# Optimization experiments

Hardware: AMD Instinct MI355X
Metric: run time of the kernel (lower is better)

Reference implementation:

```python
import jax, jax.numpy as jnp
import numpy as np

NMS_THRE = 0.4
NEG = -1e30  # sentinel for sort key of suppressed boxes


def _iou_adjacency(boxes, nms_thre):
    # boxes: [N,4] in cxcywh -> xyxy, then dense IoU >= thre adjacency (no self loops)
    cx, cy, w, h = boxes[:, 0], boxes[:, 1], boxes[:, 2], boxes[:, 3]
    x1 = cx - w / 2
    y1 = cy - h / 2
    x2 = x1 + w
    y2 = y1 + h
    b = jnp.stack([x1, y1, x2, y2], axis=-1)  # [N,4]
    area = (x2 - x1) * (y2 - y1)
    lt = jnp.maximum(b[:, None, :2], b[None, :, :2])  # [N,N,2]
    rb = jnp.minimum(b[:, None, 2:], b[None, :, 2:])
    wh = jnp.clip(rb - lt, 0.0)
    inter = wh[..., 0] * wh[..., 1]
    iou = inter / (area[:, None] + area[None, :] - inter)
    n = boxes.shape[0]
    return (iou >= nms_thre) & (~jnp.eye(n, dtype=bool))


def _greedy_suppress(valid0, adj, scores):
    # Sequential greedy NMS over candidates in descending score order.
    # valid shrinks monotonically, and valid <= valid0 always, so clearing
    # neighbors via adj row exactly matches the torch loop (which only clears
    # neighbors that were initially valid -- already-false entries are no-ops).
    order = jnp.argsort(-scores)

    def body(k, valid):
        idx = order[k]
        return jnp.where(valid[idx], valid & (~adj[idx]), valid)

    return jax.lax.fori_loop(0, scores.shape[0], body, valid0)


def _per_class(pro_c, con_c, conf_c, adj):
    # scatter_max over adjacency: max of con over neighbors (0 if no neighbors,
    # matching torch_scatter's zero-init)
    adj_con = jnp.max(jnp.where(adj, con_c[None, :], 0.0), axis=1)
    valid0 = (pro_c >= conf_c) & (pro_c >= adj_con) & (pro_c >= con_c)
    return _greedy_suppress(valid0, adj, pro_c)


def _per_image(pro, con, boxes, scale, conf_thres):
    # pro/con: [N,C]; boxes: [N,4] cxcywh; scale: scalar; conf_thres: [C]
    adj = _iou_adjacency(boxes, NMS_THRE)
    survive = jax.vmap(_per_class, in_axes=(1, 1, 0, None))(pro, con, conf_thres, adj)  # [C,N]
    b = boxes * scale
    cx, cy, w, h = b[:, 0], b[:, 1], b[:, 2], b[:, 3]
    xyxy = jnp.stack([cx - 0.5 * w, cy - 0.5 * h, cx + 0.5 * w, cy + 0.5 * h], axis=-1)  # [N,4]
    scores = pro.T  # [C,N]
    C = scores.shape[0]
    bws = jnp.concatenate(
        [jnp.broadcast_to(xyxy[None], (C,) + xyxy.shape), scores[..., None]], axis=-1
    )  # [C,N,5]
    bws = bws * survive[..., None].astype(bws.dtype)  # zero out suppressed rows
    key = jnp.where(survive, scores, NEG)
    perm = jnp.argsort(-key, axis=1)  # per-class descending score order
    bws = jnp.take_along_axis(bws, perm[..., None], axis=1)
    mask = jnp.take_along_axis(survive, perm, axis=1)
    return bws, mask


def setup_inputs() -> dict:
    key = jax.random.key(0)
    k1, k2, k3, k4 = jax.random.split(key, 4)
    B, N, C = 4, 3600, 16
    return {
        "pro_max": jax.random.uniform(k1, (B, N, C), dtype=jnp.float32),
        "con_max": jax.random.uniform(k2, (B, N, C), dtype=jnp.float32),
        "pred_boxes": jax.random.uniform(k3, (B, N, 4), dtype=jnp.float32),
        "image_scales": jax.random.uniform(k4, (B,), dtype=jnp.float32),
        "conf_thres": jnp.zeros((C,), dtype=jnp.float32),
    }


def reference(pro_max, con_max, pred_boxes, image_scales, conf_thres):
    # Returns (boxes_with_scores [B,C,N,5] sorted per class by score desc,
    #          survive_mask [B,C,N] aligned with the sorted rows).
    return jax.vmap(_per_image, in_axes=(0, 0, 0, 0, None))(
        pro_max, con_max, pred_boxes, image_scales, conf_thres
    )
```

## Files before the change

### kernel.cpp

```cpp
#include <hip/hip_runtime.h>
#include <cstdint>

typedef unsigned long long u64;
typedef unsigned int u32;

#define B_ 4
#define N_ 3600
#define C_ 16
#define NW_ 57
#define NPAD_ 3648
#define RPW_ 4
#define RPB_ 16
#define TPI_ 1596
#define HW0_ 1856
#define HW1_ 1792
#define CH_ 64
#define NTC_ 1024
#define NWVC_ 16
#define RPWGC_ 4

__global__ __launch_bounds__(256, 4) void k_adj(const float* __restrict__ boxes,
                                                u64* __restrict__ adj) {
#pragma clang fp contract(off)
    __shared__ float4 sbox[HW0_];
    const int tid  = threadIdx.x;
    const int lane = tid & 63;
    const int wv   = tid >> 6;
    const int g    = blockIdx.x;
    const int b    = g / (N_ / RPB_);
    const int rg   = g % (N_ / RPB_);
    const int r0   = rg * RPB_ + wv * RPW_;
    const int w0   = rg >> 2;
    const size_t bN = (size_t)b * N_;

    float4 bi[RPW_];
    float  ai[RPW_];
#pragma unroll
    for (int r = 0; r < RPW_; ++r) {
        const float4 bx = reinterpret_cast<const float4*>(boxes)[bN + r0 + r];
        const float x1 = bx.x - bx.z * 0.5f;
        const float y1 = bx.y - bx.w * 0.5f;
        const float x2 = x1 + bx.z;
        const float y2 = y1 + bx.w;
        bi[r] = make_float4(x1, y1, x2, y2);
        ai[r] = (x2 - x1) * (y2 - y1);
    }
    const double MID = (double)0.4f - 0x1p-26;

    u64 row[RPW_];
#pragma unroll
    for (int r = 0; r < RPW_; ++r) row[r] = 0ull;

    int jbase = 0;
    for (int h = 0; h < 2; ++h) {
        const int cnt  = h ? HW1_ : HW0_;
        const int wlo  = jbase >> 6;
        const int wcnt = cnt >> 6;
        if (w0 < wlo + wcnt) {
            const int tw0 = max(w0 - wlo, 0);
            const int jj0 = tw0 << 6;
            __syncthreads();
            for (int jj = jj0 + tid; jj < cnt; jj += 256) {
                const int j = jbase + jj;
                float x1 = 0.f, y1 = 0.f, x2 = 0.f, y2 = 0.f;
                if (j < N_) {
                    const float4 bx = reinterpret_cast<const float4*>(boxes)[bN + j];
                    x1 = bx.x - bx.z * 0.5f;
                    y1 = bx.y - bx.w * 0.5f;
                    x2 = x1 + bx.z;
                    y2 = y1 + bx.w;
                }
                sbox[jj] = make_float4(x1, y1, x2, y2);
            }
            __syncthreads();

            for (int tw = tw0; tw < wcnt; ++tw) {
                const int tglob = wlo + tw;
                const float4 bj = sbox[tw * 64 + lane];
                const float ajr = (bj.z - bj.x) * (bj.w - bj.y);
#pragma unroll
                for (int r = 0; r < RPW_; ++r) {
                    const float ltx = fmaxf(bi[r].x, bj.x);
                    const float lty = fmaxf(bi[r].y, bj.y);
                    const float rbx = fminf(bi[r].z, bj.z);
                    const float rby = fminf(bi[r].w, bj.w);
                    const float whx = fmaxf(rbx - ltx, 0.0f);
                    const float why = fmaxf(rby - lty, 0.0f);
                    const float inter = whx * why;
                    const float denom = (ai[r] + ajr) - inter;
                    const int pred = ((double)inter > MID * (double)denom);
                    const u64 m = __ballot(pred);
                    if (lane == tglob) row[r] = m;
                }
            }
        }
        jbase += cnt;
    }

#pragma unroll
    for (int r = 0; r < RPW_; ++r)
        if (lane == w0) row[r] &= ~(1ull << ((r0 + r) & 63));
#pragma unroll
    for (int r = 0; r < RPW_; ++r)
        if (lane >= w0 && lane < NW_)
            adj[(bN + r0 + r) * (size_t)NW_ + lane] = row[r];
}

__global__ __launch_bounds__(256) void k_tr(u64* __restrict__ adj,
                                            u32* __restrict__ cnt) {
    if (blockIdx.x == 0) {
        for (int x = threadIdx.x; x < B_ * C_ * 16; x += 256) cnt[x] = 0;
    }
    const int lane = threadIdx.x & 63;
    const int wv   = threadIdx.x >> 6;
    const int p    = blockIdx.x * 4 + wv;
    const int b    = p / TPI_;
    const int p2   = p % TPI_;
    int wi = (int)((1.0f + sqrtf((float)(8 * p2 + 1))) * 0.5f);
    while (wi * (wi - 1) / 2 > p2) --wi;
    while ((wi + 1) * wi / 2 <= p2) ++wi;
    const int wj = p2 - wi * (wi - 1) / 2;
    const size_t bN = (size_t)b * N_;

    u64 x = adj[(bN + wj * 64 + lane) * (size_t)NW_ + wi];

    const u64 M[6] = {0x00000000FFFFFFFFull, 0x0000FFFF0000FFFFull,
                      0x00FF00FF00FF00FFull, 0x0F0F0F0F0F0F0F0Full,
                      0x3333333333333333ull, 0x5555555555555555ull};
#pragma unroll
    for (int si = 0; si < 6; ++si) {
        const int s = 32 >> si;
        const u64 m = M[si];
        const u64 t = __shfl_xor(x, s);
        x = ((lane & s) == 0) ? ((x & m) | ((t & m) << s))
                              : ((x & ~m) | ((t & ~m) >> s));
    }
    const int rowi = wi * 64 + lane;
    if (rowi < N_)
        adj[(bN + rowi) * (size_t)NW_ + wj] = x;
}

__global__ __launch_bounds__(256) void k_acon(const u64* __restrict__ adj,
                                              const float* __restrict__ con,
                                              const float* __restrict__ pro,
                                              const float* __restrict__ conf,
                                              u64* __restrict__ cand,
                                              u32* __restrict__ cnt) {
    const int tid  = threadIdx.x;
    const int lane = tid & 63;
    const int wv   = tid >> 6;
    const int g    = blockIdx.x;
    const int b    = g / (N_ / 4);
    const int i    = (g % (N_ / 4)) * 4 + wv;
    const size_t bN = (size_t)b * N_;

    u64 w = (lane < NW_) ? adj[(bN + i) * (size_t)NW_ + lane] : 0ull;

    float cm[C_];
#pragma unroll
    for (int k = 0; k < C_; ++k) cm[k] = 0.0f;

    while (w) {
        const int bit = __builtin_ctzll(w); w &= w - 1;
        const int j   = lane * 64 + bit;
        const float4* cp = reinterpret_cast<const float4*>(con + (bN + j) * C_);
        const float4 c0 = cp[0], c1 = cp[1], c2 = cp[2], c3 = cp[3];
        cm[0]  = fmaxf(cm[0],  c0.x); cm[1]  = fmaxf(cm[1],  c0.y);
        cm[2]  = fmaxf(cm[2],  c0.z); cm[3]  = fmaxf(cm[3],  c0.w);
        cm[4]  = fmaxf(cm[4],  c1.x); cm[5]  = fmaxf(cm[5],  c1.y);
        cm[6]  = fmaxf(cm[6],  c1.z); cm[7]  = fmaxf(cm[7],  c1.w);
        cm[8]  = fmaxf(cm[8],  c2.x); cm[9]  = fmaxf(cm[9],  c2.y);
        cm[10] = fmaxf(cm[10], c2.z); cm[11] = fmaxf(cm[11], c2.w);
        cm[12] = fmaxf(cm[12], c3.x); cm[13] = fmaxf(cm[13], c3.y);
        cm[14] = fmaxf(cm[14], c3.z); cm[15] = fmaxf(cm[15], c3.w);
    }

#pragma unroll
    for (int off = 1; off < 64; off <<= 1) {
#pragma unroll
        for (int k = 0; k < C_; ++k) cm[k] = fmaxf(cm[k], __shfl_xor(cm[k], off));
    }
    if (lane == 0) {
        const float4* cp = reinterpret_cast<const float4*>(con + (bN + i) * C_);
        const float4 c0 = cp[0], c1 = cp[1], c2 = cp[2], c3 = cp[3];
        const float4* pp = reinterpret_cast<const float4*>(pro + (bN + i) * C_);
        const float4 p0 = pp[0], p1 = pp[1], p2 = pp[2], p3 = pp[3];
        const float4* fp = reinterpret_cast<const float4*>(conf);
        const float4 f0 = fp[0], f1 = fp[1], f2 = fp[2], f3 = fp[3];
        const float th[C_] = {
            fmaxf(cm[0],  c0.x), fmaxf(cm[1],  c0.y),
            fmaxf(cm[2],  c0.z), fmaxf(cm[3],  c0.w),
            fmaxf(cm[4],  c1.x), fmaxf(cm[5],  c1.y),
            fmaxf(cm[6],  c1.z), fmaxf(cm[7],  c1.w),
            fmaxf(cm[8],  c2.x), fmaxf(cm[9],  c2.y),
            fmaxf(cm[10], c2.z), fmaxf(cm[11], c2.w),
            fmaxf(cm[12], c3.x), fmaxf(cm[13], c3.y),
            fmaxf(cm[14], c3.z), fmaxf(cm[15], c3.w)};
        const float pr[C_] = {p0.x, p0.y, p0.z, p0.w, p1.x, p1.y, p1.z, p1.w,
                              p2.x, p2.y, p2.z, p2.w, p3.x, p3.y, p3.z, p3.w};
        const float cf[C_] = {f0.x, f0.y, f0.z, f0.w, f1.x, f1.y, f1.z, f1.w,
                              f2.x, f2.y, f2.z, f2.w, f3.x, f3.y, f3.z, f3.w};
#pragma unroll
        for (int k = 0; k < C_; ++k) {
            if (pr[k] >= cf[k] && pr[k] >= th[k]) {
                const u32 pb = __float_as_uint(pr[k]);
                const u32 pk = pb ^ ((pb >> 31) ? 0xFFFFFFFFu : 0x80000000u);
                const u32 pos = atomicAdd(&cnt[(b * C_ + k) * 16], 1u);
                cand[(size_t)(b * C_ + k) * N_ + pos] =
                    (((u64)(~pk)) << 32) | (u32)i;
            }
        }
    }
}

union OvT {
    u64 keys[NPAD_];
    u64 srows[2][CH_][NW_];
};

__global__ __launch_bounds__(NTC_) void k_nms_core(const u64* __restrict__ cand,
                                                   const u32* __restrict__ cnt,
                                                   const u64* __restrict__ adj,
                                                   u32* __restrict__ scnt,
                                                   u32* __restrict__ sl,
                                                   float* __restrict__ sf) {
#pragma clang fp contract(off)
    __shared__ OvT ov;
    __shared__ u32 sidx[NPAD_];
    __shared__ float sscore[NPAD_];
    __shared__ u64 sintra[CH_];
    __shared__ u64 vmask[NW_];
    __shared__ u64 s_accept;
    __shared__ u32 slist[NPAD_];
    __shared__ float slistf[NPAD_];
    __shared__ u32 s_S;
    const int tid  = threadIdx.x;
    const int lane = tid & 63;
    const int wv   = tid >> 6;
    const int bc   = blockIdx.x;
    const int b    = bc / C_;
    const size_t bN = (size_t)b * N_;

    const int T  = (int)cnt[bc * 16];
    const int TW = (T + 63) >> 6;
    for (int x = tid; x < TW * 64; x += NTC_)
        ov.keys[x] = (x < T) ? cand[(size_t)bc * N_ + x] : ~0ull;
    if (tid < NW_) vmask[tid] = 0ull;
    __syncthreads();

    for (int xp = 0; xp * NTC_ < T; ++xp) {
        const int x  = xp * NTC_ + tid;
        const u64 kx = (x < T) ? ov.keys[x] : ~0ull;
        u32 rank = 0;
        if (x < TW * 64) {
            for (int yb = 0; yb < TW; ++yb) {
                const u64 ky = ov.keys[yb * 64 + lane];
                const u32 kyl = (u32)ky, kyh = (u32)(ky >> 32);
#pragma unroll
                for (int l = 0; l < 64; ++l) {
                    const u64 kb =
                        ((u64)(u32)__builtin_amdgcn_readlane((int)kyh, l) << 32)
                      |  (u64)(u32)__builtin_amdgcn_readlane((int)kyl, l);
                    rank += (kb < kx) ? 1u : 0u;
                }
            }
        }
        if (x < T) {
            const u32 i = (u32)(kx & 0xFFFFFFFFull);
            sidx[rank] = i;
            const u32 pk = ~((u32)(kx >> 32));
            const u32 pb = (pk & 0x80000000u) ? (pk ^ 0x80000000u) : ~pk;
            sscore[rank] = __uint_as_float(pb);
            atomicOr(&vmask[i >> 6], 1ull << (i & 63));
        }
    }
    __syncthreads();

#pragma unroll
    for (int rr = 0; rr < RPWGC_; ++rr) {
        const int r = wv * RPWGC_ + rr;
        const u32 idx = (r < T) ? sidx[r] : 0u;
        if (lane < NW_)
            ov.srows[0][r][lane] = adj[(bN + idx) * (size_t)NW_ + lane];
    }
    __syncthreads();

    u32 S = 0;
    const int NCH = (T + CH_ - 1) / CH_;
    for (int ch = 0; ch < NCH; ++ch) {
        const int cur = ch & 1, nxt = cur ^ 1;
        const int c0 = ch * CH_;
        const int cn = min(CH_, T - c0);
        const int havenext = (ch + 1 < NCH);

        u64 pre[RPWGC_];
#pragma unroll
        for (int rr = 0; rr < RPWGC_; ++rr) {
            const int r = wv * RPWGC_ + rr;
            const int q = c0 + CH_ + r;
            const u32 idxn = (havenext && q < T) ? sidx[q] : 0u;
            pre[rr] = (havenext && lane < NW_)
                        ? adj[(bN + idxn) * (size_t)NW_ + lane] : 0ull;
        }
#pragma unroll
        for (int rr = 0; rr < RPWGC_; ++rr) {
            const int r = wv * RPWGC_ + rr;
            const u32 idxr = (c0 + r < T) ? sidx[c0 + r] : 0u;
            const u64 rj = ov.srows[cur][lane][idxr >> 6];
            const u64 ib = __ballot((lane < cn) && ((rj >> (idxr & 63)) & 1ull));
            if (lane == 0) sintra[r] = ib;
        }
        __syncthreads();

        if (wv == 0) {
            const u32 idxme = (c0 + lane < T) ? sidx[c0 + lane] : 0u;
            const u64 vm = vmask[idxme >> 6];
            u64 cv = __ballot((lane < cn) && ((vm >> (idxme & 63)) & 1ull));
            const u64 iv = sintra[lane];
            const u64 below = (1ull << lane) - 1ull;
            u64 accept = 0ull;
            while (cv) {
                const int ok = ((cv >> lane) & 1ull) &&
                               ((iv & below & cv) == 0ull);
                const u64 ar = __ballot(ok);
                u64 sup = ok ? iv : 0ull;
#pragma unroll
                for (int off = 1; off < 64; off <<= 1)
                    sup |= __shfl_xor(sup, off);
                accept |= ar;
                cv &= ~(ar | sup);
            }
            if (lane == 0) s_accept = accept;
            if ((accept >> lane) & 1ull) {
                const u32 pos = S + (u32)__popcll(accept & below);
                slist[pos]  = idxme;
                slistf[pos] = sscore[c0 + lane];
            }
            S += (u32)__popcll(accept);
        }
        __syncthreads();

        const u64 ac = s_accept;
        u64 acc = 0ull;
#pragma unroll
        for (int rr = 0; rr < RPWGC_; ++rr) {
            const int r = wv * RPWGC_ + rr;
            if ((ac >> r) & 1ull)
                acc |= ov.srows[cur][r][min(lane, NW_ - 1)];
        }
        if (lane < NW_ && acc)
            atomicAnd(&vmask[lane], ~acc);
        if (havenext) {
#pragma unroll
            for (int rr = 0; rr < RPWGC_; ++rr) {
                const int r = wv * RPWGC_ + rr;
                if (lane < NW_) ov.srows[nxt][r][lane] = pre[rr];
            }
        }
        __syncthreads();
    }
    if (wv == 0 && lane == 0) { s_S = S; scnt[bc] = S; }
    __syncthreads();

    const int Sf = (int)s_S;
    for (int r = tid; r < Sf; r += NTC_) {
        sl[(size_t)bc * N_ + r] = slist[r];
        sf[(size_t)bc * N_ + r] = slistf[r];
    }
}

__global__ __launch_bounds__(512) void k_out(const u32* __restrict__ scnt,
                                             const u32* __restrict__ sl,
                                             const float* __restrict__ sf,
                                             const float* __restrict__ boxes,
                                             const float* __restrict__ scales,
                                             float* __restrict__ out) {
#pragma clang fp contract(off)
    const int x = blockIdx.x * 512 + threadIdx.x;
    if (x >= B_ * C_ * N_) return;
    const int bc = x / N_;
    const int r  = x - bc * N_;
    const int b  = bc / C_;
    const int S  = (int)scnt[bc];

    float o0 = 0.f, o1 = 0.f, o2 = 0.f, o3 = 0.f, o4 = 0.f, mk = 0.f;
    if (r < S) {
        const int idx = (int)sl[(size_t)bc * N_ + r];
        const float4 bx =
            reinterpret_cast<const float4*>(boxes)[(size_t)b * N_ + idx];
        const float s = scales[b];
        const float scx = bx.x * s, scy = bx.y * s;
        const float sw  = bx.z * s, sh  = bx.w * s;
        o0 = scx - 0.5f * sw;
        o1 = scy - 0.5f * sh;
        o2 = scx + 0.5f * sw;
        o3 = scy + 0.5f * sh;
        o4 = sf[(size_t)bc * N_ + r];
        mk = 1.0f;
    }
    float* o = out + (size_t)x * 5;
    o[0] = o0; o[1] = o1; o[2] = o2; o[3] = o3; o[4] = o4;
    out[(size_t)B_ * C_ * N_ * 5 + x] = mk;
}

extern "C" void kernel_launch(void* const* d_in, const int* in_sizes, int n_in,
                              void* d_out, int out_size, void* d_ws, size_t ws_size,
                              hipStream_t stream) {
    const float* pro    = (const float*)d_in[0];
    const float* con    = (const float*)d_in[1];
    const float* boxes  = (const float*)d_in[2];
    const float* scales = (const float*)d_in[3];
    const float* conf   = (const float*)d_in[4];

    char* ws = (char*)d_ws;
    u64* adj = (u64*)ws;
    size_t off = (size_t)B_ * N_ * NW_ * sizeof(u64);
    u64* cand = (u64*)(ws + off);
    off += (size_t)B_ * C_ * N_ * sizeof(u64);
    u32* cnt = (u32*)(ws + off);
    off += (size_t)B_ * C_ * 16 * sizeof(u32);
    u32* scnt = (u32*)(ws + off);
    off += (size_t)B_ * C_ * sizeof(u32);
    u32* sl = (u32*)(ws + off);
    off += (size_t)B_ * C_ * N_ * sizeof(u32);
    float* sf = (float*)(ws + off);

    k_adj     <<<B_ * N_ / RPB_, 256, 0, stream>>>(boxes, adj);
    k_tr      <<<B_ * TPI_ / 4,  256, 0, stream>>>(adj, cnt);
    k_acon    <<<B_ * N_ / 4,    256, 0, stream>>>(adj, con, pro, conf, cand, cnt);
    k_nms_core<<<B_ * C_,        NTC_, 0, stream>>>(cand, cnt, adj, scnt, sl, sf);
    k_out     <<<450,            512, 0, stream>>>(scnt, sl, sf, boxes, scales,
                                                   (float*)d_out);
}
```

Baseline: 157.0 us.

## Compact neighbor list in LDS and parallelize class max across lanes

In k_acon, each wave now turns its adjacency bitmask into a compact list of neighbor indices in shared memory, using a popcount prefix scan across lanes. The neighbor max of con is then computed with lane = class (16 classes x 4 groups) using coalesced scalar loads, instead of per-lane loops that each read all 16 classes. This replaces the 16-wide register reduction over all 64 lanes with two shuffles, and the final per-class candidate emission is spread across 16 lanes instead of lane 0 doing all classes. The cost is a 28.8KB shared array per block, which can limit occupancy, plus a __syncthreads.

New measurement: 164.0 us. 1.04x slower.

```diff
diff --git a/kernel.cpp b/kernel.cpp
--- a/kernel.cpp
+++ b/kernel.cpp
@@ -3,6 +3,7 @@
 
 typedef unsigned long long u64;
 typedef unsigned int u32;
+typedef unsigned short u16;
 
 #define B_ 4
 #define N_ 3600
@@ -146,6 +147,7 @@
                                               const float* __restrict__ conf,
                                               u64* __restrict__ cand,
                                               u32* __restrict__ cnt) {
+    __shared__ u16 nl[4][N_];
     const int tid  = threadIdx.x;
     const int lane = tid & 63;
     const int wv   = tid >> 6;
@@ -154,61 +156,44 @@
     const int i    = (g % (N_ / 4)) * 4 + wv;
     const size_t bN = (size_t)b * N_;
 
-    u64 w = (lane < NW_) ? adj[(bN + i) * (size_t)NW_ + lane] : 0ull;
-
-    float cm[C_];
-#pragma unroll
-    for (int k = 0; k < C_; ++k) cm[k] = 0.0f;
-
-    while (w) {
-        const int bit = __builtin_ctzll(w); w &= w - 1;
-        const int j   = lane * 64 + bit;
-        const float4* cp = reinterpret_cast<const float4*>(con + (bN + j) * C_);
-        const float4 c0 = cp[0], c1 = cp[1], c2 = cp[2], c3 = cp[3];
-        cm[0]  = fmaxf(cm[0],  c0.x); cm[1]  = fmaxf(cm[1],  c0.y);
-        cm[2]  = fmaxf(cm[2],  c0.z); cm[3]  = fmaxf(cm[3],  c0.w);
-        cm[4]  = fmaxf(cm[4],  c1.x); cm[5]  = fmaxf(cm[5],  c1.y);
-        cm[6]  = fmaxf(cm[6],  c1.z); cm[7]  = fmaxf(cm[7],  c1.w);
-        cm[8]  = fmaxf(cm[8],  c2.x); cm[9]  = fmaxf(cm[9],  c2.y);
-        cm[10] = fmaxf(cm[10], c2.z); cm[11] = fmaxf(cm[11], c2.w);
-        cm[12] = fmaxf(cm[12], c3.x); cm[13] = fmaxf(cm[13], c3.y);
-        cm[14] = fmaxf(cm[14], c3.z); cm[15] = fmaxf(cm[15], c3.w);
-    }
-
-#pragma unroll
-    for (int off = 1; off < 64; off <<= 1) {
-#pragma unroll
-        for (int k = 0; k < C_; ++k) cm[k] = fmaxf(cm[k], __shfl_xor(cm[k], off));
-    }
-    if (lane == 0) {
-        const float4* cp = reinterpret_cast<const float4*>(con + (bN + i) * C_);
-        const float4 c0 = cp[0], c1 = cp[1], c2 = cp[2], c3 = cp[3];
-        const float4* pp = reinterpret_cast<const float4*>(pro + (bN + i) * C_);
-        const float4 p0 = pp[0], p1 = pp[1], p2 = pp[2], p3 = pp[3];
-        const float4* fp = reinterpret_cast<const float4*>(conf);
-        const float4 f0 = fp[0], f1 = fp[1], f2 = fp[2], f3 = fp[3];
-        const float th[C_] = {
-            fmaxf(cm[0],  c0.x), fmaxf(cm[1],  c0.y),
-            fmaxf(cm[2],  c0.z), fmaxf(cm[3],  c0.w),
-            fmaxf(cm[4],  c1.x), fmaxf(cm[5],  c1.y),
-            fmaxf(cm[6],  c1.z), fmaxf(cm[7],  c1.w),
-            fmaxf(cm[8],  c2.x), fmaxf(cm[9],  c2.y),
-            fmaxf(cm[10], c2.z), fmaxf(cm[11], c2.w),
-            fmaxf(cm[12], c3.x), fmaxf(cm[13], c3.y),
-            fmaxf(cm[14], c3.z), fmaxf(cm[15], c3.w)};
-        const float pr[C_] = {p0.x, p0.y, p0.z, p0.w, p1.x, p1.y, p1.z, p1.w,
-                              p2.x, p2.y, p2.z, p2.w, p3.x, p3.y, p3.z, p3.w};
-        const float cf[C_] = {f0.x, f0.y, f0.z, f0.w, f1.x, f1.y, f1.z, f1.w,
-                              f2.x, f2.y, f2.z, f2.w, f3.x, f3.y, f3.z, f3.w};
-#pragma unroll
-        for (int k = 0; k < C_; ++k) {
-            if (pr[k] >= cf[k] && pr[k] >= th[k]) {
-                const u32 pb = __float_as_uint(pr[k]);
-                const u32 pk = pb ^ ((pb >> 31) ? 0xFFFFFFFFu : 0x80000000u);
-                const u32 pos = atomicAdd(&cnt[(b * C_ + k) * 16], 1u);
-                cand[(size_t)(b * C_ + k) * N_ + pos] =
-                    (((u64)(~pk)) << 32) | (u32)i;
-            }
+    const u64 w = (lane < NW_) ? adj[(bN + i) * (size_t)NW_ + lane] : 0ull;
+
+    const u32 c = (u32)__popcll(w);
+    u32 off = c;
+#pragma unroll
+    for (int d = 1; d < 64; d <<= 1) {
+        const u32 t = (u32)__shfl_up((int)off, d);
+        if (lane >= d) off += t;
+    }
+    const u32 TN = (u32)__shfl((int)off, 63);
+    u32 p = off - c;
+    u64 ww = w;
+    while (ww) {
+        const int bit = __builtin_ctzll(ww); ww &= ww - 1;
+        nl[wv][p++] = (u16)(lane * 64 + bit);
+    }
+    __syncthreads();
+
+    const int k   = lane & 15;
+    const int grp = lane >> 4;
+    float cm = 0.0f;
+    for (u32 n = (u32)grp; n < TN; n += 4) {
+        const int j = (int)nl[wv][n];
+        cm = fmaxf(cm, con[(bN + j) * C_ + k]);
+    }
+    cm = fmaxf(cm, __shfl_xor(cm, 16));
+    cm = fmaxf(cm, __shfl_xor(cm, 32));
+
+    if (lane < C_) {
+        const float ci = con[(bN + i) * C_ + k];
+        const float th = fmaxf(cm, ci);
+        const float pv = pro[(bN + i) * C_ + k];
+        if (pv >= conf[k] && pv >= th) {
+            const u32 pb = __float_as_uint(pv);
+            const u32 pk = pb ^ ((pb >> 31) ? 0xFFFFFFFFu : 0x80000000u);
+            const u32 pos = atomicAdd(&cnt[(b * C_ + k) * 16], 1u);
+            cand[(size_t)(b * C_ + k) * N_ + pos] =
+                (((u64)(~pk)) << 32) | (u32)i;
         }
     }
 }
```
